# Kernel optimization log

Hardware: AMD Instinct MI355X
Metric: run time of the kernel (lower is better)

The kernel has to match this reference:

```python
import jax, jax.numpy as jnp
import numpy as np

F, N, D, K = 32, 4096, 64, 512
COMMITMENT_COST = 0.25


def setup_inputs() -> dict:
    key = jax.random.key(0)
    k1, k2 = jax.random.split(key)
    inputs = jax.random.normal(k1, (F, N, D), dtype=jnp.float32)
    # GlorotUniform on weight shape [F, D, K]
    limit = float(np.sqrt(6.0 / (D + K)))
    w = jax.random.uniform(k2, (F, D, K), dtype=jnp.float32, minval=-limit, maxval=limit)
    return {"inputs": inputs, "w": w}


def reference(inputs, w):
    # inputs: [F, N, D], w: [F, D, K]
    distances = (
        jnp.sum(inputs ** 2, axis=2, keepdims=True)
        - 2.0 * jnp.einsum('fnd,fdk->fnk', inputs, w)
        + jnp.sum(w ** 2, axis=1, keepdims=True)
    )
    enc_idx = jnp.argmin(distances, axis=2)  # [F, N]
    w_t = jnp.swapaxes(w, 1, 2)  # [F, K, D]
    quantized = jnp.take_along_axis(w_t, enc_idx[:, :, None], axis=1)  # [F, N, D]
    e_latent_loss = jnp.mean((jax.lax.stop_gradient(quantized) - inputs) ** 2)
    q_latent_loss = jnp.mean((quantized - jax.lax.stop_gradient(inputs)) ** 2)
    loss = q_latent_loss + COMMITMENT_COST * e_latent_loss
    # straight-through estimator
    output = inputs + jax.lax.stop_gradient(quantized - inputs)
    return output, loss
```

## Files before the change

### kernel.cpp

```cpp
#include <hip/hip_runtime.h>
#include <math.h>

#define NF 32
#define NN 4096
#define ND 64
#define NK 512

#define LOSS_SCALE (1.25f / (float)(NF * NN * ND))
#define TAU 6e-4f

#define NPARTIAL (NF * NN * 4 / 256)

typedef short bf16x8 __attribute__((ext_vector_type(8)));
typedef float f32x4 __attribute__((ext_vector_type(4)));

static __device__ __forceinline__ unsigned short f2bf_rne(float f) {
    unsigned int u = __float_as_uint(f);
    u += 0x7FFFu + ((u >> 16) & 1u);
    return (unsigned short)(u >> 16);
}
static __device__ __forceinline__ float bf2f(unsigned short h) {
    return __uint_as_float(((unsigned int)h) << 16);
}

static __device__ __forceinline__ void gload_lds16(const void* g, void* l) {
    __builtin_amdgcn_global_load_lds(
        (const __attribute__((address_space(1))) unsigned int*)g,
        (__attribute__((address_space(3))) unsigned int*)l, 16, 0, 0);
}

__global__ __launch_bounds__(256)
void vq_prep_w(const float* __restrict__ w, float* __restrict__ wt,
               unsigned short* __restrict__ wh, unsigned short* __restrict__ wl,
               float* __restrict__ w2h) {
    const int gid = blockIdx.x * 256 + threadIdx.x;
    const int dc = gid & 7;
    const int k  = (gid >> 3) & (NK - 1);
    const int f  = gid >> 12;
    const float* __restrict__ wf = w + (size_t)f * ND * NK;
    const size_t rowo = ((size_t)f * NK + k) * ND + dc * 8;

    float v[8];
    unsigned short hh[8], ll[8];
    float s = 0.0f;
#pragma unroll
    for (int j = 0; j < 8; ++j) {
        v[j] = wf[(dc * 8 + j) * NK + k];
        s = fmaf(v[j], v[j], s);
        hh[j] = f2bf_rne(v[j]);
        ll[j] = f2bf_rne(v[j] - bf2f(hh[j]));
    }
    *(float4*)(wt + rowo)     = make_float4(v[0], v[1], v[2], v[3]);
    *(float4*)(wt + rowo + 4) = make_float4(v[4], v[5], v[6], v[7]);
    *(ushort4*)(wh + rowo)     = make_ushort4(hh[0], hh[1], hh[2], hh[3]);
    *(ushort4*)(wh + rowo + 4) = make_ushort4(hh[4], hh[5], hh[6], hh[7]);
    *(ushort4*)(wl + rowo)     = make_ushort4(ll[0], ll[1], ll[2], ll[3]);
    *(ushort4*)(wl + rowo + 4) = make_ushort4(ll[4], ll[5], ll[6], ll[7]);

    s += __shfl_xor(s, 1, 64);
    s += __shfl_xor(s, 2, 64);
    s += __shfl_xor(s, 4, 64);
    if (dc == 0) w2h[f * NK + k] = 0.5f * s;
}

__global__ __launch_bounds__(256, 2)
void vq_argmin(const float* __restrict__ x_in,
               const unsigned short* __restrict__ wh,
               const unsigned short* __restrict__ wl,
               const float* __restrict__ w2h,
               unsigned int* __restrict__ keys,
               unsigned char* __restrict__ flags) {
    const int b    = blockIdx.x;
    const int g8   = b >> 3;
    const int f    = (b & 7) * 4 + (g8 >> 4);
    const int xt   = g8 & 15;
    const int tid  = threadIdx.x;
    const int wave = tid >> 6;
    const int lane = tid & 63;
    const int lc   = lane & 15;
    const int q    = lane >> 4;
    const int n0   = xt * 256 + wave * 64;

    __shared__ float nw2s[NK];
    __shared__ __align__(16) unsigned short bstage[2][8192];

    for (int t = tid; t < NK; t += 256) nw2s[t] = -w2h[f * NK + t];

    bf16x8 ah[4][2], al[4][2];
    const float* __restrict__ xbase = x_in + ((size_t)f * NN + n0 + lc) * ND;
#pragma unroll
    for (int mt = 0; mt < 4; ++mt) {
#pragma unroll
        for (int s = 0; s < 2; ++s) {
            const float* p = xbase + mt * 16 * ND + s * 32 + q * 8;
            float4 u0 = *(const float4*)(p);
            float4 u1 = *(const float4*)(p + 4);
            float xv[8] = {u0.x, u0.y, u0.z, u0.w, u1.x, u1.y, u1.z, u1.w};
            bf16x8 h, l;
#pragma unroll
            for (int j = 0; j < 8; ++j) {
                unsigned short hb = f2bf_rne(xv[j]);
                unsigned short lb = f2bf_rne(xv[j] - bf2f(hb));
                h[j] = (short)hb;
                l[j] = (short)lb;
            }
            ah[mt][s] = h;
            al[mt][s] = l;
        }
    }

    const unsigned short* __restrict__ whf = wh + (size_t)f * NK * ND;
    const unsigned short* __restrict__ wlf = wl + (size_t)f * NK * ND;

    float m1[16], m2[16];
    int idx[16];
#pragma unroll
    for (int ri = 0; ri < 16; ++ri) { m1[ri] = INFINITY; m2[ri] = INFINITY; idx[ri] = 0; }

#define STAGE(st, pb) do {                                                  \
    _Pragma("unroll")                                                       \
    for (int rep = 0; rep < 4; ++rep) {                                     \
        const int c  = wave * 4 + rep;                                      \
        const int tl = c >> 2;                                              \
        const int sg = (c >> 1) & 1;                                        \
        const unsigned short* src = ((c & 1) ? wlf : whf) +                 \
            (size_t)((st) * 64 + tl * 16 + lc) * ND + q * 8 + sg * 32;      \
        gload_lds16(src, &bstage[pb][c * 512]);                             \
    }                                                                       \
} while (0)

    STAGE(0, 0);

    for (int st = 0; st < 8; ++st) {
        __syncthreads();
        if (st < 7) STAGE(st + 1, (st + 1) & 1);
        const unsigned short* __restrict__ bb = &bstage[st & 1][0];

#pragma unroll
        for (int tl = 0; tl < 4; ++tl) {
            const int col = st * 64 + tl * 16 + lc;
            bf16x8 bh0 = *(const bf16x8*)(bb + (tl * 4 + 0) * 512 + lane * 8);
            bf16x8 bl0 = *(const bf16x8*)(bb + (tl * 4 + 1) * 512 + lane * 8);
            bf16x8 bh1 = *(const bf16x8*)(bb + (tl * 4 + 2) * 512 + lane * 8);
            bf16x8 bl1 = *(const bf16x8*)(bb + (tl * 4 + 3) * 512 + lane * 8);
            const float nw2 = nw2s[col];
#pragma unroll
            for (int mt = 0; mt < 4; ++mt) {
                f32x4 c = {nw2, nw2, nw2, nw2};
                c = __builtin_amdgcn_mfma_f32_16x16x32_bf16(ah[mt][0], bh0, c, 0, 0, 0);
                c = __builtin_amdgcn_mfma_f32_16x16x32_bf16(ah[mt][1], bh1, c, 0, 0, 0);
                c = __builtin_amdgcn_mfma_f32_16x16x32_bf16(ah[mt][0], bl0, c, 0, 0, 0);
                c = __builtin_amdgcn_mfma_f32_16x16x32_bf16(ah[mt][1], bl1, c, 0, 0, 0);
                c = __builtin_amdgcn_mfma_f32_16x16x32_bf16(al[mt][0], bh0, c, 0, 0, 0);
                c = __builtin_amdgcn_mfma_f32_16x16x32_bf16(al[mt][1], bh1, c, 0, 0, 0);
#pragma unroll
                for (int r = 0; r < 4; ++r) {
                    const int ri = mt * 4 + r;
                    const float sc = -c[r];
                    const bool lt = sc < m1[ri];
                    m2[ri]  = __builtin_amdgcn_fmed3f(sc, m1[ri], m2[ri]);
                    m1[ri]  = lt ? sc : m1[ri];
                    idx[ri] = lt ? col : idx[ri];
                }
            }
        }
    }

#pragma unroll
    for (int ri = 0; ri < 16; ++ri) {
        float a1 = m1[ri], a2 = m2[ri];
        int ai = idx[ri];
#pragma unroll
        for (int off = 1; off < 16; off <<= 1) {
            const float b1 = __shfl_xor(a1, off, 64);
            const float b2 = __shfl_xor(a2, off, 64);
            const int   bi = __shfl_xor(ai, off, 64);
            const float hi = fmaxf(a1, b1);
            const bool take = (b1 < a1) || (b1 == a1 && bi < ai);
            a1 = take ? b1 : a1;
            ai = take ? bi : ai;
            a2 = fminf(fminf(a2, b2), hi);
        }
        m1[ri] = a1; m2[ri] = a2; idx[ri] = ai;
    }

    if (lc == 0) {
#pragma unroll
        for (int mt = 0; mt < 4; ++mt) {
            const int g = f * NN + n0 + mt * 16 + q * 4;
            uint4 kv;
            kv.x = (unsigned int)idx[mt * 4 + 0];
            kv.y = (unsigned int)idx[mt * 4 + 1];
            kv.z = (unsigned int)idx[mt * 4 + 2];
            kv.w = (unsigned int)idx[mt * 4 + 3];
            *(uint4*)(keys + g) = kv;
            uchar4 fl;
            fl.x = (m2[mt * 4 + 0] - m1[mt * 4 + 0] < TAU) ? 1 : 0;
            fl.y = (m2[mt * 4 + 1] - m1[mt * 4 + 1] < TAU) ? 1 : 0;
            fl.z = (m2[mt * 4 + 2] - m1[mt * 4 + 2] < TAU) ? 1 : 0;
            fl.w = (m2[mt * 4 + 3] - m1[mt * 4 + 3] < TAU) ? 1 : 0;
            *(uchar4*)(flags + g) = fl;
        }
    }
}

__global__ __launch_bounds__(256)
void vq_rescue(const float* __restrict__ x_in, const float* __restrict__ wt,
               const float* __restrict__ w2h,
               const unsigned char* __restrict__ flags,
               unsigned int* __restrict__ keys) {
    const int lane = threadIdx.x & 63;
    const int wid  = (blockIdx.x * 256 + threadIdx.x) >> 6;
    const int base = wid * 64;

    unsigned long long m = __ballot(flags[base + lane] != 0);
    while (m) {
        const int r = __ffsll(m) - 1;
        m &= m - 1;
        const int g = base + r;
        const int f = g >> 12;
        const float* __restrict__ xr  = x_in + (size_t)g * ND;
        const float* __restrict__ wtf = wt + (size_t)f * NK * ND;
        unsigned long long best = 0xFFFFFFFFFFFFFFFFULL;
#pragma unroll 1
        for (int j = 0; j < 8; ++j) {
            const int col = j * 64 + lane;
            const float* __restrict__ wr = wtf + (size_t)col * ND;
            float t = w2h[f * NK + col];
#pragma unroll
            for (int d = 0; d < ND; d += 4) {
                float4 xv = *(const float4*)(xr + d);
                float4 wv = *(const float4*)(wr + d);
                t = fmaf(-xv.x, wv.x, t);
                t = fmaf(-xv.y, wv.y, t);
                t = fmaf(-xv.z, wv.z, t);
                t = fmaf(-xv.w, wv.w, t);
            }
            unsigned int u = __float_as_uint(t);
            u ^= (unsigned int)((int)u >> 31) | 0x80000000u;
            const unsigned long long key =
                ((unsigned long long)u << 32) | (unsigned int)col;
            best = key < best ? key : best;
        }
#pragma unroll
        for (int off = 32; off > 0; off >>= 1) {
            const unsigned long long o = __shfl_xor(best, off, 64);
            best = o < best ? o : best;
        }
        if (lane == 0) keys[g] = (unsigned int)(best & 0xFFFFFFFFULL);
    }
}

__global__ __launch_bounds__(256)
void vq_gather(const float* __restrict__ x_in, const float* __restrict__ wt,
               const unsigned int* __restrict__ keys, float* __restrict__ out,
               float* __restrict__ partial) {
    const int gid = blockIdx.x * 256 + threadIdx.x;
    const int row = gid >> 2;
    const int c   = (gid & 3) * 16;
    const int f   = row >> 12;
    const unsigned int k = keys[row];

    const float* __restrict__ q16 = wt + ((size_t)f * NK + k) * ND + c;
    const float* __restrict__ x16 = x_in + (size_t)row * ND + c;
    float* __restrict__ o16       = out + (size_t)row * ND + c;

    float lsum = 0.0f;
#pragma unroll
    for (int j = 0; j < 4; ++j) {
        float4 qv = *(const float4*)(q16 + 4 * j);
        float4 xv = *(const float4*)(x16 + 4 * j);
        const float dx0 = qv.x - xv.x;
        const float dx1 = qv.y - xv.y;
        const float dx2 = qv.z - xv.z;
        const float dx3 = qv.w - xv.w;
        lsum = fmaf(dx0, dx0, lsum);
        lsum = fmaf(dx1, dx1, lsum);
        lsum = fmaf(dx2, dx2, lsum);
        lsum = fmaf(dx3, dx3, lsum);
        *(float4*)(o16 + 4 * j) = qv;
    }

#pragma unroll
    for (int off = 32; off > 0; off >>= 1) {
        lsum += __shfl_down(lsum, off, 64);
    }
    __shared__ float wsum[4];
    if ((threadIdx.x & 63) == 0) wsum[threadIdx.x >> 6] = lsum;
    __syncthreads();
    if (threadIdx.x == 0) {
        partial[blockIdx.x] = wsum[0] + wsum[1] + wsum[2] + wsum[3];
    }
}

__global__ __launch_bounds__(256)
void vq_loss_final(const float* __restrict__ partial, float* __restrict__ loss) {
    float s = 0.0f;
    for (int i = threadIdx.x; i < NPARTIAL; i += 256) s += partial[i];
#pragma unroll
    for (int off = 32; off > 0; off >>= 1) s += __shfl_down(s, off, 64);
    __shared__ float wsum[4];
    if ((threadIdx.x & 63) == 0) wsum[threadIdx.x >> 6] = s;
    __syncthreads();
    if (threadIdx.x == 0) {
        *loss = (wsum[0] + wsum[1] + wsum[2] + wsum[3]) * LOSS_SCALE;
    }
}

extern "C" void kernel_launch(void* const* d_in, const int* in_sizes, int n_in,
                              void* d_out, int out_size, void* d_ws, size_t ws_size,
                              hipStream_t stream) {
    const float* x_in = (const float*)d_in[0];
    const float* w    = (const float*)d_in[1];
    float* out        = (float*)d_out;

    float* wt  = (float*)d_ws;
    float* w2h = wt + (size_t)NF * NK * ND;
    unsigned short* wh = (unsigned short*)(w2h + NF * NK);
    unsigned short* wl = wh + (size_t)NF * NK * ND;
    unsigned int* keys = (unsigned int*)(wl + (size_t)NF * NK * ND);
    unsigned char* flags = (unsigned char*)(keys + (size_t)NF * NN);
    float* partial = (float*)(flags + (size_t)NF * NN);

    float* loss_slot = out + (size_t)NF * NN * ND;

    vq_prep_w<<<NF * NK * 8 / 256, 256, 0, stream>>>(w, wt, wh, wl, w2h);

    vq_argmin<<<NF * NN / 256, 256, 0, stream>>>(x_in, wh, wl, w2h, keys, flags);

    vq_rescue<<<NF * NN / 64 / 4, 256, 0, stream>>>(x_in, wt, w2h, flags, keys);

    vq_gather<<<NF * NN * 4 / 256, 256, 0, stream>>>(x_in, wt, keys, out, partial);

    vq_loss_final<<<1, 256, 0, stream>>>(partial, loss_slot);
}
```

Before: 170.6 us.

## Split codebook columns across waves and merge argmin through shared memory

The argmin kernel now gives each block 64 rows, and its four waves each scan a different quarter of the 512 codebook columns instead of each wave scanning all columns for its own 64 rows. Codebook tiles are read directly from global memory into registers rather than double-buffered into LDS with async loads. Per-wave minima are merged in shared memory at the end. This launches four times as many blocks for more parallelism and removes the LDS staging barriers, at the cost of an extra reduction step and less reuse of codebook data within a block, since the x tile is loaded once per block.

```diff
diff --git a/kernel.cpp b/kernel.cpp
--- a/kernel.cpp
+++ b/kernel.cpp
@@ -21,12 +21,6 @@
 }
 static __device__ __forceinline__ float bf2f(unsigned short h) {
     return __uint_as_float(((unsigned int)h) << 16);
-}
-
-static __device__ __forceinline__ void gload_lds16(const void* g, void* l) {
-    __builtin_amdgcn_global_load_lds(
-        (const __attribute__((address_space(1))) unsigned int*)g,
-        (__attribute__((address_space(3))) unsigned int*)l, 16, 0, 0);
 }
 
 __global__ __launch_bounds__(256)
@@ -71,18 +65,19 @@
                unsigned int* __restrict__ keys,
                unsigned char* __restrict__ flags) {
     const int b    = blockIdx.x;
-    const int g8   = b >> 3;
-    const int f    = (b & 7) * 4 + (g8 >> 4);
-    const int xt   = g8 & 15;
+    const int xcd  = b & 7;
+    const int j    = b >> 3;
+    const int f    = xcd * 4 + (j & 3);
+    const int n0   = (j >> 2) * 64;
     const int tid  = threadIdx.x;
     const int wave = tid >> 6;
     const int lane = tid & 63;
     const int lc   = lane & 15;
-    const int q    = lane >> 4;
-    const int n0   = xt * 256 + wave * 64;
+    const int kq   = lane >> 4;
 
     __shared__ float nw2s[NK];
-    __shared__ __align__(16) unsigned short bstage[2][8192];
+    __shared__ float mrg1[4][64], mrg2[4][64];
+    __shared__ int   mrgi[4][64];
 
     for (int t = tid; t < NK; t += 256) nw2s[t] = -w2h[f * NK + t];
 
@@ -92,17 +87,17 @@
     for (int mt = 0; mt < 4; ++mt) {
 #pragma unroll
         for (int s = 0; s < 2; ++s) {
-            const float* p = xbase + mt * 16 * ND + s * 32 + q * 8;
+            const float* p = xbase + mt * 16 * ND + s * 32 + kq * 8;
             float4 u0 = *(const float4*)(p);
             float4 u1 = *(const float4*)(p + 4);
             float xv[8] = {u0.x, u0.y, u0.z, u0.w, u1.x, u1.y, u1.z, u1.w};
             bf16x8 h, l;
 #pragma unroll
-            for (int j = 0; j < 8; ++j) {
-                unsigned short hb = f2bf_rne(xv[j]);
-                unsigned short lb = f2bf_rne(xv[j] - bf2f(hb));
-                h[j] = (short)hb;
-                l[j] = (short)lb;
+            for (int jj = 0; jj < 8; ++jj) {
+                unsigned short hb = f2bf_rne(xv[jj]);
+                unsigned short lb = f2bf_rne(xv[jj] - bf2f(hb));
+                h[jj] = (short)hb;
+                l[jj] = (short)lb;
             }
             ah[mt][s] = h;
             al[mt][s] = l;
@@ -111,57 +106,42 @@
 
     const unsigned short* __restrict__ whf = wh + (size_t)f * NK * ND;
     const unsigned short* __restrict__ wlf = wl + (size_t)f * NK * ND;
+    const int cq = wave * 128;
 
     float m1[16], m2[16];
     int idx[16];
 #pragma unroll
     for (int ri = 0; ri < 16; ++ri) { m1[ri] = INFINITY; m2[ri] = INFINITY; idx[ri] = 0; }
 
-#define STAGE(st, pb) do {                                                  \
-    _Pragma("unroll")                                                       \
-    for (int rep = 0; rep < 4; ++rep) {                                     \
-        const int c  = wave * 4 + rep;                                      \
-        const int tl = c >> 2;                                              \
-        const int sg = (c >> 1) & 1;                                        \
-        const unsigned short* src = ((c & 1) ? wlf : whf) +                 \
-            (size_t)((st) * 64 + tl * 16 + lc) * ND + q * 8 + sg * 32;      \
-        gload_lds16(src, &bstage[pb][c * 512]);                             \
-    }                                                                       \
-} while (0)
-
-    STAGE(0, 0);
-
-    for (int st = 0; st < 8; ++st) {
-        __syncthreads();
-        if (st < 7) STAGE(st + 1, (st + 1) & 1);
-        const unsigned short* __restrict__ bb = &bstage[st & 1][0];
-
-#pragma unroll
-        for (int tl = 0; tl < 4; ++tl) {
-            const int col = st * 64 + tl * 16 + lc;
-            bf16x8 bh0 = *(const bf16x8*)(bb + (tl * 4 + 0) * 512 + lane * 8);
-            bf16x8 bl0 = *(const bf16x8*)(bb + (tl * 4 + 1) * 512 + lane * 8);
-            bf16x8 bh1 = *(const bf16x8*)(bb + (tl * 4 + 2) * 512 + lane * 8);
-            bf16x8 bl1 = *(const bf16x8*)(bb + (tl * 4 + 3) * 512 + lane * 8);
-            const float nw2 = nw2s[col];
-#pragma unroll
-            for (int mt = 0; mt < 4; ++mt) {
-                f32x4 c = {nw2, nw2, nw2, nw2};
-                c = __builtin_amdgcn_mfma_f32_16x16x32_bf16(ah[mt][0], bh0, c, 0, 0, 0);
-                c = __builtin_amdgcn_mfma_f32_16x16x32_bf16(ah[mt][1], bh1, c, 0, 0, 0);
-                c = __builtin_amdgcn_mfma_f32_16x16x32_bf16(ah[mt][0], bl0, c, 0, 0, 0);
-                c = __builtin_amdgcn_mfma_f32_16x16x32_bf16(ah[mt][1], bl1, c, 0, 0, 0);
-                c = __builtin_amdgcn_mfma_f32_16x16x32_bf16(al[mt][0], bh0, c, 0, 0, 0);
-                c = __builtin_amdgcn_mfma_f32_16x16x32_bf16(al[mt][1], bh1, c, 0, 0, 0);
-#pragma unroll
-                for (int r = 0; r < 4; ++r) {
-                    const int ri = mt * 4 + r;
-                    const float sc = -c[r];
-                    const bool lt = sc < m1[ri];
-                    m2[ri]  = __builtin_amdgcn_fmed3f(sc, m1[ri], m2[ri]);
-                    m1[ri]  = lt ? sc : m1[ri];
-                    idx[ri] = lt ? col : idx[ri];
-                }
+    __syncthreads();
+
+#pragma unroll 2
+    for (int tl = 0; tl < 8; ++tl) {
+        const int colbase = cq + tl * 16;
+        const int col = colbase + lc;
+        const size_t bo = (size_t)col * ND + kq * 8;
+        bf16x8 bh0 = *(const bf16x8*)(whf + bo);
+        bf16x8 bh1 = *(const bf16x8*)(whf + bo + 32);
+        bf16x8 bl0 = *(const bf16x8*)(wlf + bo);
+        bf16x8 bl1 = *(const bf16x8*)(wlf + bo + 32);
+        const float nw2 = nw2s[col];
+#pragma unroll
+        for (int mt = 0; mt < 4; ++mt) {
+            f32x4 c = {nw2, nw2, nw2, nw2};
+            c = __builtin_amdgcn_mfma_f32_16x16x32_bf16(ah[mt][0], bh0, c, 0, 0, 0);
+            c = __builtin_amdgcn_mfma_f32_16x16x32_bf16(ah[mt][1], bh1, c, 0, 0, 0);
+            c = __builtin_amdgcn_mfma_f32_16x16x32_bf16(ah[mt][0], bl0, c, 0, 0, 0);
+            c = __builtin_amdgcn_mfma_f32_16x16x32_bf16(ah[mt][1], bl1, c, 0, 0, 0);
+            c = __builtin_amdgcn_mfma_f32_16x16x32_bf16(al[mt][0], bh0, c, 0, 0, 0);
+            c = __builtin_amdgcn_mfma_f32_16x16x32_bf16(al[mt][1], bh1, c, 0, 0, 0);
+#pragma unroll
+            for (int r = 0; r < 4; ++r) {
+                const int ri = mt * 4 + r;
+                const float sc = -c[r];
+                const bool lt = sc < m1[ri];
+                m2[ri]  = __builtin_amdgcn_fmed3f(sc, m1[ri], m2[ri]);
+                m1[ri]  = lt ? sc : m1[ri];
+                idx[ri] = lt ? col : idx[ri];
             }
         }
     }
@@ -186,21 +166,34 @@
 
     if (lc == 0) {
 #pragma unroll
-        for (int mt = 0; mt < 4; ++mt) {
-            const int g = f * NN + n0 + mt * 16 + q * 4;
-            uint4 kv;
-            kv.x = (unsigned int)idx[mt * 4 + 0];
-            kv.y = (unsigned int)idx[mt * 4 + 1];
-            kv.z = (unsigned int)idx[mt * 4 + 2];
-            kv.w = (unsigned int)idx[mt * 4 + 3];
-            *(uint4*)(keys + g) = kv;
-            uchar4 fl;
-            fl.x = (m2[mt * 4 + 0] - m1[mt * 4 + 0] < TAU) ? 1 : 0;
-            fl.y = (m2[mt * 4 + 1] - m1[mt * 4 + 1] < TAU) ? 1 : 0;
-            fl.z = (m2[mt * 4 + 2] - m1[mt * 4 + 2] < TAU) ? 1 : 0;
-            fl.w = (m2[mt * 4 + 3] - m1[mt * 4 + 3] < TAU) ? 1 : 0;
-            *(uchar4*)(flags + g) = fl;
-        }
+        for (int ri = 0; ri < 16; ++ri) {
+            const int mt = ri >> 2, r = ri & 3;
+            const int row = mt * 16 + kq * 4 + r;
+            mrg1[wave][row] = m1[ri];
+            mrg2[wave][row] = m2[ri];
+            mrgi[wave][row] = idx[ri];
+        }
+    }
+    __syncthreads();
+
+    if (tid < 64) {
+        const int row = tid;
+        float a1 = mrg1[0][row], a2 = mrg2[0][row];
+        int ai = mrgi[0][row];
+#pragma unroll
+        for (int wq = 1; wq < 4; ++wq) {
+            const float b1 = mrg1[wq][row];
+            const float b2 = mrg2[wq][row];
+            const int   bi = mrgi[wq][row];
+            const float hi = fmaxf(a1, b1);
+            const bool take = b1 < a1;
+            a2 = fminf(fminf(a2, b2), hi);
+            a1 = take ? b1 : a1;
+            ai = take ? bi : ai;
+        }
+        const int g = f * NN + n0 + row;
+        keys[g]  = (unsigned int)ai;
+        flags[g] = (a2 - a1 < TAU) ? 1 : 0;
     }
 }
 
@@ -223,8 +216,8 @@
         const float* __restrict__ wtf = wt + (size_t)f * NK * ND;
         unsigned long long best = 0xFFFFFFFFFFFFFFFFULL;
 #pragma unroll 1
-        for (int j = 0; j < 8; ++j) {
-            const int col = j * 64 + lane;
+        for (int jj = 0; jj < 8; ++jj) {
+            const int col = jj * 64 + lane;
             const float* __restrict__ wr = wtf + (size_t)col * ND;
             float t = w2h[f * NK + col];
 #pragma unroll
@@ -267,9 +260,9 @@
 
     float lsum = 0.0f;
 #pragma unroll
-    for (int j = 0; j < 4; ++j) {
-        float4 qv = *(const float4*)(q16 + 4 * j);
-        float4 xv = *(const float4*)(x16 + 4 * j);
+    for (int jj = 0; jj < 4; ++jj) {
+        float4 qv = *(const float4*)(q16 + 4 * jj);
+        float4 xv = *(const float4*)(x16 + 4 * jj);
         const float dx0 = qv.x - xv.x;
         const float dx1 = qv.y - xv.y;
         const float dx2 = qv.z - xv.z;
@@ -278,7 +271,7 @@
         lsum = fmaf(dx1, dx1, lsum);
         lsum = fmaf(dx2, dx2, lsum);
         lsum = fmaf(dx3, dx3, lsum);
-        *(float4*)(o16 + 4 * j) = qv;
+        *(float4*)(o16 + 4 * jj) = qv;
     }
 
 #pragma unroll
@@ -326,7 +319,7 @@
 
     vq_prep_w<<<NF * NK * 8 / 256, 256, 0, stream>>>(w, wt, wh, wl, w2h);
 
-    vq_argmin<<<NF * NN / 256, 256, 0, stream>>>(x_in, wh, wl, w2h, keys, flags);
+    vq_argmin<<<NF * NN / 64, 256, 0, stream>>>(x_in, wh, wl, w2h, keys, flags);
 
     vq_rescue<<<NF * NN / 64 / 4, 256, 0, stream>>>(x_in, wt, w2h, flags, keys);
 
```

After: 198.2 us. 1.16x slower.

## Pack column index into distance bits and halve argmin tile for occupancy

Applied to the files above, without the earlier changes.

The argmin kernel now gives each wave 32 rows instead of 64, launches twice as many blocks, halves the LDS staging per stage, and raises the launch-bounds occupancy hint from 2 to 4. It negates x before the bf16 split so the accumulator starts from +w2 and holds the distance directly. It also packs the 9-bit column index into the low mantissa bits of the score, so a single fminf/fmed3 tracks both value and index, which removes the separate index registers and simplifies the cross-lane reduction. The mantissa truncation costs distance precision, and TAU is raised to compensate, so more rows are flagged for the exact rescue pass.

```diff
diff --git a/kernel.cpp b/kernel.cpp
--- a/kernel.cpp
+++ b/kernel.cpp
@@ -7,7 +7,7 @@
 #define NK 512
 
 #define LOSS_SCALE (1.25f / (float)(NF * NN * ND))
-#define TAU 6e-4f
+#define TAU 1.5e-3f
 
 #define NPARTIAL (NF * NN * 4 / 256)
 
@@ -63,7 +63,7 @@
     if (dc == 0) w2h[f * NK + k] = 0.5f * s;
 }
 
-__global__ __launch_bounds__(256, 2)
+__global__ __launch_bounds__(256, 4)
 void vq_argmin(const float* __restrict__ x_in,
                const unsigned short* __restrict__ wh,
                const unsigned short* __restrict__ wl,
@@ -71,38 +71,38 @@
                unsigned int* __restrict__ keys,
                unsigned char* __restrict__ flags) {
     const int b    = blockIdx.x;
-    const int g8   = b >> 3;
-    const int f    = (b & 7) * 4 + (g8 >> 4);
-    const int xt   = g8 & 15;
+    const int j    = b >> 3;
+    const int f    = (b & 7) * 4 + (j & 3);
+    const int xt   = j >> 2;
     const int tid  = threadIdx.x;
     const int wave = tid >> 6;
     const int lane = tid & 63;
     const int lc   = lane & 15;
     const int q    = lane >> 4;
-    const int n0   = xt * 256 + wave * 64;
-
-    __shared__ float nw2s[NK];
-    __shared__ __align__(16) unsigned short bstage[2][8192];
-
-    for (int t = tid; t < NK; t += 256) nw2s[t] = -w2h[f * NK + t];
-
-    bf16x8 ah[4][2], al[4][2];
+    const int n0   = xt * 128 + wave * 32;
+
+    __shared__ float w2s[NK];
+    __shared__ __align__(16) unsigned short bstage[2][4096];
+
+    for (int t = tid; t < NK; t += 256) w2s[t] = w2h[f * NK + t];
+
+    bf16x8 ah[2][2], al[2][2];
     const float* __restrict__ xbase = x_in + ((size_t)f * NN + n0 + lc) * ND;
 #pragma unroll
-    for (int mt = 0; mt < 4; ++mt) {
+    for (int mt = 0; mt < 2; ++mt) {
 #pragma unroll
         for (int s = 0; s < 2; ++s) {
             const float* p = xbase + mt * 16 * ND + s * 32 + q * 8;
             float4 u0 = *(const float4*)(p);
             float4 u1 = *(const float4*)(p + 4);
-            float xv[8] = {u0.x, u0.y, u0.z, u0.w, u1.x, u1.y, u1.z, u1.w};
+            float xv[8] = {-u0.x, -u0.y, -u0.z, -u0.w, -u1.x, -u1.y, -u1.z, -u1.w};
             bf16x8 h, l;
 #pragma unroll
-            for (int j = 0; j < 8; ++j) {
-                unsigned short hb = f2bf_rne(xv[j]);
-                unsigned short lb = f2bf_rne(xv[j] - bf2f(hb));
-                h[j] = (short)hb;
-                l[j] = (short)lb;
+            for (int jj = 0; jj < 8; ++jj) {
+                unsigned short hb = f2bf_rne(xv[jj]);
+                unsigned short lb = f2bf_rne(xv[jj] - bf2f(hb));
+                h[jj] = (short)hb;
+                l[jj] = (short)lb;
             }
             ah[mt][s] = h;
             al[mt][s] = l;
@@ -112,41 +112,40 @@
     const unsigned short* __restrict__ whf = wh + (size_t)f * NK * ND;
     const unsigned short* __restrict__ wlf = wl + (size_t)f * NK * ND;
 
-    float m1[16], m2[16];
-    int idx[16];
-#pragma unroll
-    for (int ri = 0; ri < 16; ++ri) { m1[ri] = INFINITY; m2[ri] = INFINITY; idx[ri] = 0; }
+    float m1[8], m2[8];
+#pragma unroll
+    for (int ri = 0; ri < 8; ++ri) { m1[ri] = INFINITY; m2[ri] = INFINITY; }
 
 #define STAGE(st, pb) do {                                                  \
     _Pragma("unroll")                                                       \
-    for (int rep = 0; rep < 4; ++rep) {                                     \
-        const int c  = wave * 4 + rep;                                      \
+    for (int rep = 0; rep < 2; ++rep) {                                     \
+        const int c  = wave * 2 + rep;                                      \
         const int tl = c >> 2;                                              \
         const int sg = (c >> 1) & 1;                                        \
         const unsigned short* src = ((c & 1) ? wlf : whf) +                 \
-            (size_t)((st) * 64 + tl * 16 + lc) * ND + q * 8 + sg * 32;      \
+            (size_t)((st) * 32 + tl * 16 + lc) * ND + q * 8 + sg * 32;      \
         gload_lds16(src, &bstage[pb][c * 512]);                             \
     }                                                                       \
 } while (0)
 
     STAGE(0, 0);
 
-    for (int st = 0; st < 8; ++st) {
+    for (int st = 0; st < 16; ++st) {
         __syncthreads();
-        if (st < 7) STAGE(st + 1, (st + 1) & 1);
+        if (st < 15) STAGE(st + 1, (st + 1) & 1);
         const unsigned short* __restrict__ bb = &bstage[st & 1][0];
 
 #pragma unroll
-        for (int tl = 0; tl < 4; ++tl) {
-            const int col = st * 64 + tl * 16 + lc;
+        for (int tl = 0; tl < 2; ++tl) {
+            const int col = st * 32 + tl * 16 + lc;
             bf16x8 bh0 = *(const bf16x8*)(bb + (tl * 4 + 0) * 512 + lane * 8);
             bf16x8 bl0 = *(const bf16x8*)(bb + (tl * 4 + 1) * 512 + lane * 8);
             bf16x8 bh1 = *(const bf16x8*)(bb + (tl * 4 + 2) * 512 + lane * 8);
             bf16x8 bl1 = *(const bf16x8*)(bb + (tl * 4 + 3) * 512 + lane * 8);
-            const float nw2 = nw2s[col];
-#pragma unroll
-            for (int mt = 0; mt < 4; ++mt) {
-                f32x4 c = {nw2, nw2, nw2, nw2};
+            const float w2 = w2s[col];
+#pragma unroll
+            for (int mt = 0; mt < 2; ++mt) {
+                f32x4 c = {w2, w2, w2, w2};
                 c = __builtin_amdgcn_mfma_f32_16x16x32_bf16(ah[mt][0], bh0, c, 0, 0, 0);
                 c = __builtin_amdgcn_mfma_f32_16x16x32_bf16(ah[mt][1], bh1, c, 0, 0, 0);
                 c = __builtin_amdgcn_mfma_f32_16x16x32_bf16(ah[mt][0], bl0, c, 0, 0, 0);
@@ -156,49 +155,45 @@
 #pragma unroll
                 for (int r = 0; r < 4; ++r) {
                     const int ri = mt * 4 + r;
-                    const float sc = -c[r];
-                    const bool lt = sc < m1[ri];
-                    m2[ri]  = __builtin_amdgcn_fmed3f(sc, m1[ri], m2[ri]);
-                    m1[ri]  = lt ? sc : m1[ri];
-                    idx[ri] = lt ? col : idx[ri];
+                    const float key = __uint_as_float(
+                        (__float_as_uint(c[r]) & 0xFFFFFE00u) | (unsigned int)col);
+                    m2[ri] = __builtin_amdgcn_fmed3f(key, m1[ri], m2[ri]);
+                    m1[ri] = fminf(key, m1[ri]);
                 }
             }
         }
     }
 
 #pragma unroll
-    for (int ri = 0; ri < 16; ++ri) {
+    for (int ri = 0; ri < 8; ++ri) {
         float a1 = m1[ri], a2 = m2[ri];
-        int ai = idx[ri];
 #pragma unroll
         for (int off = 1; off < 16; off <<= 1) {
             const float b1 = __shfl_xor(a1, off, 64);
             const float b2 = __shfl_xor(a2, off, 64);
-            const int   bi = __shfl_xor(ai, off, 64);
-            const float hi = fmaxf(a1, b1);
-            const bool take = (b1 < a1) || (b1 == a1 && bi < ai);
-            a1 = take ? b1 : a1;
-            ai = take ? bi : ai;
-            a2 = fminf(fminf(a2, b2), hi);
-        }
-        m1[ri] = a1; m2[ri] = a2; idx[ri] = ai;
+            a2 = fminf(fminf(a2, b2), fmaxf(a1, b1));
+            a1 = fminf(a1, b1);
+        }
+        m1[ri] = a1; m2[ri] = a2;
     }
 
     if (lc == 0) {
 #pragma unroll
-        for (int mt = 0; mt < 4; ++mt) {
+        for (int mt = 0; mt < 2; ++mt) {
             const int g = f * NN + n0 + mt * 16 + q * 4;
             uint4 kv;
-            kv.x = (unsigned int)idx[mt * 4 + 0];
-            kv.y = (unsigned int)idx[mt * 4 + 1];
-            kv.z = (unsigned int)idx[mt * 4 + 2];
-            kv.w = (unsigned int)idx[mt * 4 + 3];
+            uchar4 fl;
+#pragma unroll
+            for (int r = 0; r < 4; ++r) {
+                const int ri = mt * 4 + r;
+                const unsigned int u1 = __float_as_uint(m1[ri]);
+                const unsigned int u2 = __float_as_uint(m2[ri]);
+                const float s1 = __uint_as_float(u1 & 0xFFFFFE00u);
+                const float s2 = __uint_as_float(u2 & 0xFFFFFE00u);
+                ((unsigned int*)&kv)[r] = u1 & 0x1FFu;
+                ((unsigned char*)&fl)[r] = (s2 - s1 < TAU) ? 1 : 0;
+            }
             *(uint4*)(keys + g) = kv;
-            uchar4 fl;
-            fl.x = (m2[mt * 4 + 0] - m1[mt * 4 + 0] < TAU) ? 1 : 0;
-            fl.y = (m2[mt * 4 + 1] - m1[mt * 4 + 1] < TAU) ? 1 : 0;
-            fl.z = (m2[mt * 4 + 2] - m1[mt * 4 + 2] < TAU) ? 1 : 0;
-            fl.w = (m2[mt * 4 + 3] - m1[mt * 4 + 3] < TAU) ? 1 : 0;
             *(uchar4*)(flags + g) = fl;
         }
     }
@@ -223,8 +218,8 @@
         const float* __restrict__ wtf = wt + (size_t)f * NK * ND;
         unsigned long long best = 0xFFFFFFFFFFFFFFFFULL;
 #pragma unroll 1
-        for (int j = 0; j < 8; ++j) {
-            const int col = j * 64 + lane;
+        for (int jj = 0; jj < 8; ++jj) {
+            const int col = jj * 64 + lane;
             const float* __restrict__ wr = wtf + (size_t)col * ND;
             float t = w2h[f * NK + col];
 #pragma unroll
@@ -267,9 +262,9 @@
 
     float lsum = 0.0f;
 #pragma unroll
-    for (int j = 0; j < 4; ++j) {
-        float4 qv = *(const float4*)(q16 + 4 * j);
-        float4 xv = *(const float4*)(x16 + 4 * j);
+    for (int jj = 0; jj < 4; ++jj) {
+        float4 qv = *(const float4*)(q16 + 4 * jj);
+        float4 xv = *(const float4*)(x16 + 4 * jj);
         const float dx0 = qv.x - xv.x;
         const float dx1 = qv.y - xv.y;
         const float dx2 = qv.z - xv.z;
@@ -278,7 +273,7 @@
         lsum = fmaf(dx1, dx1, lsum);
         lsum = fmaf(dx2, dx2, lsum);
         lsum = fmaf(dx3, dx3, lsum);
-        *(float4*)(o16 + 4 * j) = qv;
+        *(float4*)(o16 + 4 * jj) = qv;
     }
 
 #pragma unroll
@@ -326,7 +321,7 @@
 
     vq_prep_w<<<NF * NK * 8 / 256, 256, 0, stream>>>(w, wt, wh, wl, w2h);
 
-    vq_argmin<<<NF * NN / 256, 256, 0, stream>>>(x_in, wh, wl, w2h, keys, flags);
+    vq_argmin<<<NF * NN / 128, 256, 0, stream>>>(x_in, wh, wl, w2h, keys, flags);
 
     vq_rescue<<<NF * NN / 64 / 4, 256, 0, stream>>>(x_in, wt, w2h, flags, keys);
 
```

New measurement: 187.2 us. 9.8% more time.
